# Performance work log

Measured on AMD Instinct MI355X. Metric: run time of the kernel, lower is better.

Reference implementation:

```python
import jax, jax.numpy as jnp
import numpy as np
from jax import lax

B, T, I, H = 8192, 512, 3, 25  # batch, seq_len, input_size, hidden_size


def setup_inputs() -> dict:
    key = jax.random.key(0)
    ks = jax.random.split(key, 4)
    x = jax.random.normal(ks[0], (B, T, I), dtype=jnp.float32)
    # xavier-uniform-ish scale for w_ih, orthogonal-ish (plain normal here) for w_hh
    w_ih = jax.random.normal(ks[1], (4 * H, I), dtype=jnp.float32) * 0.5
    w_hh = jax.random.normal(ks[2], (4 * H, H), dtype=jnp.float32) * 0.2
    b_ih = jnp.zeros((4 * H,), dtype=jnp.float32)
    # PyTorch init in module: forget-gate bias (second quarter) set to 1 on each bias
    b_ih = b_ih.at[H:2 * H].set(1.0)
    b_hh = jnp.zeros((4 * H,), dtype=jnp.float32)
    b_hh = b_hh.at[H:2 * H].set(1.0)
    w_lin = jax.random.normal(ks[3], (1, H), dtype=jnp.float32) * 0.3
    b_lin = jnp.zeros((1,), dtype=jnp.float32)
    return {"x": x, "w_ih": w_ih, "w_hh": w_hh, "b_ih": b_ih, "b_hh": b_hh,
            "w_lin": w_lin, "b_lin": b_lin}


def _lstm_last_h(x, w_ih, w_hh, b_ih, b_hh):
    # x: [B, T, I]; returns final hidden state h_T: [B, H]
    b = b_ih + b_hh  # [4H]
    xT = jnp.swapaxes(x, 0, 1)  # [T, B, I]

    def step(carry, x_t):
        h, c = carry
        gates = x_t @ w_ih.T + h @ w_hh.T + b  # [B, 4H]
        i, f, g, o = jnp.split(gates, 4, axis=-1)  # PyTorch gate order i,f,g,o
        i = jax.nn.sigmoid(i)
        f = jax.nn.sigmoid(f)
        g = jnp.tanh(g)
        o = jax.nn.sigmoid(o)
        c = f * c + i * g
        h = o * jnp.tanh(c)
        return (h, c), None

    h0 = jnp.zeros((x.shape[0], w_hh.shape[1]), dtype=x.dtype)
    (h, _), _ = lax.scan(step, (h0, h0), xT)
    return h


def reference(x, w_ih, w_hh, b_ih, b_hh, w_lin, b_lin):
    h_last = _lstm_last_h(x, w_ih, w_hh, b_ih, b_hh)  # [B, H]
    return h_last @ w_lin.T + b_lin  # [B, 1]
```

## Files before the change

kernel.cpp:

```cpp
#include <hip/hip_runtime.h>
#include <hip/hip_bf16.h>


#define TSTEPS 512
#define ISZ 3
#define HSZ 25

typedef __attribute__((ext_vector_type(8))) short bf16x8;
typedef __attribute__((ext_vector_type(4))) float f32x4;
typedef __attribute__((ext_vector_type(4))) int i32x4;
typedef __attribute__((ext_vector_type(2))) float v2f;

__device__ __forceinline__ unsigned short bf16_bits(float v) {
    return __builtin_bit_cast(unsigned short, __float2bfloat16(v));
}
__device__ __forceinline__ unsigned int pack_bf16(float lo, float hi) {
    return ((unsigned int)bf16_bits(hi) << 16) | (unsigned int)bf16_bits(lo);
}
__device__ __forceinline__ v2f rcp2(v2f v) {
    return (v2f){__builtin_amdgcn_rcpf(v.x), __builtin_amdgcn_rcpf(v.y)};
}

__global__ __launch_bounds__(256, 2) void lstm_mfma(
    const float* __restrict__ x,
    const float* __restrict__ w_ih,
    const float* __restrict__ w_hh,
    const float* __restrict__ b_ih,
    const float* __restrict__ b_hh,
    const float* __restrict__ w_lin,
    const float* __restrict__ b_lin,
    float* __restrict__ out)
{
    __shared__ short hb[2][768];
    __shared__ float outred[4][16];

    const int tid  = threadIdx.x;
    const int w    = tid >> 6;
    const int lane = tid & 63;
    const int n    = lane & 15;
    const int q    = lane >> 4;
    const int b0   = blockIdx.x * 16;

    const float K1 = 1.442695040888963f;
    const float K2 = 2.885390081777927f;

    for (int i = tid; i < 2 * 768; i += 256) ((short*)hb)[i] = 0;

    bf16x8 afA, afB;
    {
        const int g = n & 3, us = n >> 2;
        const int uA = 4 * w + us;
        const int uB = 4 * (w + 4) + us;
        #pragma unroll
        for (int j = 0; j < 8; ++j) {
            const int k = q * 8 + j;
            float vA = 0.f, vB = 0.f;
            {
                const int orow = g * HSZ + uA;
                if (k < ISZ)            vA = w_ih[orow * ISZ + k];
                else if (k == ISZ)      vA = b_ih[orow] + b_hh[orow];
                else if (k < 4 + HSZ)   vA = w_hh[orow * HSZ + (k - 4)];
                vA *= (g == 2) ? -K2 : -K1;
            }
            if (uB < HSZ) {
                const int orow = g * HSZ + uB;
                if (k < ISZ)            vB = w_ih[orow * ISZ + k];
                else if (k == ISZ)      vB = b_ih[orow] + b_hh[orow];
                else if (k < 4 + HSZ)   vB = w_hh[orow * HSZ + (k - 4)];
                vB *= (g == 2) ? -K2 : -K1;
            }
            afA[j] = (short)bf16_bits(vA);
            afB[j] = (short)bf16_bits(vB);
        }
    }

    const int uwA = 4 * w + q;
    const int uwB = 4 * (w + 4) + q;
    const int kwA = uwA + 4, kwB = uwB + 4;
    const int woffA = (kwA >> 3) * 128 + n * 8 + (kwA & 7);
    const int woffB = (kwB >> 3) * 128 + n * 8 + (kwB & 7);
    const int rdoff = lane * 8;

    v2f c = {0.f, 0.f}, h = {0.f, 0.f};

    const float* __restrict__ xg = x + (size_t)(b0 + n) * (TSTEPS * ISZ);
    float4 a0 = ((const float4*)xg)[0];
    float4 a1 = ((const float4*)xg)[1];
    float4 a2 = ((const float4*)xg)[2];

    __syncthreads();

    auto step = [&](int rp, float x0, float x1, float x2) {
        bf16x8 frag = *(const bf16x8*)&hb[rp][rdoff];
        i32x4 fi = __builtin_bit_cast(i32x4, frag);
        const int px0 = (int)pack_bf16(x0, x1);
        const int px1 = (int)pack_bf16(x2, 1.0f);
        fi[0] = (q == 0) ? px0 : fi[0];
        fi[1] = (q == 0) ? px1 : fi[1];
        frag = __builtin_bit_cast(bf16x8, fi);

        const f32x4 zc = {0.f, 0.f, 0.f, 0.f};
        const f32x4 aA = __builtin_amdgcn_mfma_f32_16x16x32_bf16(afA, frag, zc, 0, 0, 0);
        const f32x4 aB = __builtin_amdgcn_mfma_f32_16x16x32_bf16(afB, frag, zc, 0, 0, 0);

        const v2f e0 = {__builtin_amdgcn_exp2f(aA[0]), __builtin_amdgcn_exp2f(aB[0])};
        const v2f e1 = {__builtin_amdgcn_exp2f(aA[1]), __builtin_amdgcn_exp2f(aB[1])};
        const v2f e2 = {__builtin_amdgcn_exp2f(fminf(aA[2], 126.f)),
                        __builtin_amdgcn_exp2f(fminf(aB[2], 126.f))};
        const v2f e3 = {__builtin_amdgcn_exp2f(aA[3]), __builtin_amdgcn_exp2f(aB[3])};
        const v2f one = {1.f, 1.f};
        const v2f s0 = e0 + one, s1 = e1 + one, s2 = e2 + one, m2 = one - e2;
        const v2f p02 = s0 * s2;
        const v2f num = c * p02 + m2 * s1;
        const v2f den = p02 * s1;
        c = num * rcp2(den);
        const v2f ec = {__builtin_amdgcn_exp2f(fminf(-K2 * c.x, 126.f)),
                        __builtin_amdgcn_exp2f(fminf(-K2 * c.y, 126.f))};
        const v2f hden = (e3 + one) * (ec + one);
        h = (one - ec) * rcp2(hden);

        const int wp = rp ^ 1;
        hb[wp][woffA] = (short)bf16_bits(h.x);
        hb[wp][woffB] = (short)bf16_bits(h.y);
        asm volatile("s_waitcnt lgkmcnt(0)" ::: "memory");
        __builtin_amdgcn_s_barrier();
    };

    #pragma unroll 1
    for (int g = 0; g < 128; g += 2) {
        const float4* __restrict__ p1 =
            (const float4*)(xg + (size_t)((g + 1 < 128 ? g + 1 : 127) * 12));
        const float4 n0 = p1[0], n1 = p1[1], n2 = p1[2];
        step(0, a0.x, a0.y, a0.z);
        step(1, a0.w, a1.x, a1.y);
        step(0, a1.z, a1.w, a2.x);
        step(1, a2.y, a2.z, a2.w);
        const float4* __restrict__ p2 =
            (const float4*)(xg + (size_t)((g + 2 < 128 ? g + 2 : 127) * 12));
        a0 = p2[0]; a1 = p2[1]; a2 = p2[2];
        step(0, n0.x, n0.y, n0.z);
        step(1, n0.w, n1.x, n1.y);
        step(0, n1.z, n1.w, n2.x);
        step(1, n2.y, n2.z, n2.w);
    }

    const float wlA = (uwA < HSZ) ? w_lin[uwA] : 0.f;
    const float wlB = (uwB < HSZ) ? w_lin[uwB] : 0.f;
    float v = wlA * h.x + wlB * h.y;
    v += __shfl_xor(v, 16);
    v += __shfl_xor(v, 32);
    if (lane < 16) outred[w][lane] = v;
    __syncthreads();
    if (tid < 16) {
        float s = b_lin[0];
        #pragma unroll
        for (int k2 = 0; k2 < 4; ++k2) s += outred[k2][tid];
        out[b0 + tid] = s;
    }
}

extern "C" void kernel_launch(void* const* d_in, const int* in_sizes, int n_in,
                              void* d_out, int out_size, void* d_ws, size_t ws_size,
                              hipStream_t stream) {
    const float* x     = (const float*)d_in[0];
    const float* w_ih  = (const float*)d_in[1];
    const float* w_hh  = (const float*)d_in[2];
    const float* b_ih  = (const float*)d_in[3];
    const float* b_hh  = (const float*)d_in[4];
    const float* w_lin = (const float*)d_in[5];
    const float* b_lin = (const float*)d_in[6];
    float* out = (float*)d_out;

    lstm_mfma<<<8192 / 16, 256, 0, stream>>>(x, w_ih, w_hh, b_ih, b_hh,
                                             w_lin, b_lin, out);
}
```

Before: 257.5 us.

## Interleave two independent batch chains per block to hide recurrence latency

Each block now handles 32 batch rows as two independent 16-row LSTM chains, interleaving their MFMA and activation work between shared barriers. This halves the number of barriers per unit of work and gives the scheduler independent instructions to cover the serial dependency latency of each step. It halves the grid to 256 blocks, sets launch bounds to one block per SM, and requests 90KB of dynamic shared memory, apparently to force single-block occupancy. That cuts available wave parallelism on a 256-CU device.

```diff
diff --git a/kernel.cpp b/kernel.cpp
--- a/kernel.cpp
+++ b/kernel.cpp
@@ -21,7 +21,7 @@
     return (v2f){__builtin_amdgcn_rcpf(v.x), __builtin_amdgcn_rcpf(v.y)};
 }
 
-__global__ __launch_bounds__(256, 2) void lstm_mfma(
+__global__ __launch_bounds__(256, 1) void lstm_mfma(
     const float* __restrict__ x,
     const float* __restrict__ w_ih,
     const float* __restrict__ w_hh,
@@ -31,20 +31,20 @@
     const float* __restrict__ b_lin,
     float* __restrict__ out)
 {
-    __shared__ short hb[2][768];
-    __shared__ float outred[4][16];
+    __shared__ short hb[2][2][768];
+    __shared__ float outred[4][2][16];
 
     const int tid  = threadIdx.x;
     const int w    = tid >> 6;
     const int lane = tid & 63;
     const int n    = lane & 15;
     const int q    = lane >> 4;
-    const int b0   = blockIdx.x * 16;
+    const int b0   = blockIdx.x * 32;
 
     const float K1 = 1.442695040888963f;
     const float K2 = 2.885390081777927f;
 
-    for (int i = tid; i < 2 * 768; i += 256) ((short*)hb)[i] = 0;
+    for (int i = tid; i < 384; i += 256) ((int4*)hb)[i] = (int4){0, 0, 0, 0};
 
     bf16x8 afA, afB;
     {
@@ -81,17 +81,23 @@
     const int woffB = (kwB >> 3) * 128 + n * 8 + (kwB & 7);
     const int rdoff = lane * 8;
 
-    v2f c = {0.f, 0.f}, h = {0.f, 0.f};
+    v2f c0 = {0.f, 0.f}, h0 = {0.f, 0.f};
+    v2f c1 = {0.f, 0.f}, h1 = {0.f, 0.f};
 
-    const float* __restrict__ xg = x + (size_t)(b0 + n) * (TSTEPS * ISZ);
-    float4 a0 = ((const float4*)xg)[0];
-    float4 a1 = ((const float4*)xg)[1];
-    float4 a2 = ((const float4*)xg)[2];
+    const float* __restrict__ xg0 = x + (size_t)(b0 + n) * (TSTEPS * ISZ);
+    const float* __restrict__ xg1 = x + (size_t)(b0 + 16 + n) * (TSTEPS * ISZ);
+    float4 A0 = ((const float4*)xg0)[0];
+    float4 A1 = ((const float4*)xg0)[1];
+    float4 A2 = ((const float4*)xg0)[2];
+    float4 B0 = ((const float4*)xg1)[0];
+    float4 B1 = ((const float4*)xg1)[1];
+    float4 B2 = ((const float4*)xg1)[2];
 
     __syncthreads();
 
-    auto step = [&](int rp, float x0, float x1, float x2) {
-        bf16x8 frag = *(const bf16x8*)&hb[rp][rdoff];
+    auto chainstep = [&](short (&buf)[2][768], int rp, v2f& c, v2f& h,
+                         float x0, float x1, float x2) {
+        bf16x8 frag = *(const bf16x8*)&buf[rp][rdoff];
         i32x4 fi = __builtin_bit_cast(i32x4, frag);
         const int px0 = (int)pack_bf16(x0, x1);
         const int px1 = (int)pack_bf16(x2, 1.0f);
@@ -120,42 +126,59 @@
         h = (one - ec) * rcp2(hden);
 
         const int wp = rp ^ 1;
-        hb[wp][woffA] = (short)bf16_bits(h.x);
-        hb[wp][woffB] = (short)bf16_bits(h.y);
+        buf[wp][woffA] = (short)bf16_bits(h.x);
+        buf[wp][woffB] = (short)bf16_bits(h.y);
+    };
+
+    auto step2 = [&](int rp, float ax0, float ax1, float ax2,
+                     float bx0, float bx1, float bx2) {
+        chainstep(hb[0], rp, c0, h0, ax0, ax1, ax2);
+        chainstep(hb[1], rp, c1, h1, bx0, bx1, bx2);
         asm volatile("s_waitcnt lgkmcnt(0)" ::: "memory");
         __builtin_amdgcn_s_barrier();
     };
 
     #pragma unroll 1
     for (int g = 0; g < 128; g += 2) {
-        const float4* __restrict__ p1 =
-            (const float4*)(xg + (size_t)((g + 1 < 128 ? g + 1 : 127) * 12));
-        const float4 n0 = p1[0], n1 = p1[1], n2 = p1[2];
-        step(0, a0.x, a0.y, a0.z);
-        step(1, a0.w, a1.x, a1.y);
-        step(0, a1.z, a1.w, a2.x);
-        step(1, a2.y, a2.z, a2.w);
-        const float4* __restrict__ p2 =
-            (const float4*)(xg + (size_t)((g + 2 < 128 ? g + 2 : 127) * 12));
-        a0 = p2[0]; a1 = p2[1]; a2 = p2[2];
-        step(0, n0.x, n0.y, n0.z);
-        step(1, n0.w, n1.x, n1.y);
-        step(0, n1.z, n1.w, n2.x);
-        step(1, n2.y, n2.z, n2.w);
+        const int gp1 = (g + 1 < 128) ? g + 1 : 127;
+        const float4* __restrict__ pA1 = (const float4*)(xg0 + (size_t)gp1 * 12);
+        const float4* __restrict__ pB1 = (const float4*)(xg1 + (size_t)gp1 * 12);
+        const float4 nA0 = pA1[0], nA1 = pA1[1], nA2 = pA1[2];
+        const float4 nB0 = pB1[0], nB1 = pB1[1], nB2 = pB1[2];
+        step2(0, A0.x, A0.y, A0.z, B0.x, B0.y, B0.z);
+        step2(1, A0.w, A1.x, A1.y, B0.w, B1.x, B1.y);
+        step2(0, A1.z, A1.w, A2.x, B1.z, B1.w, B2.x);
+        step2(1, A2.y, A2.z, A2.w, B2.y, B2.z, B2.w);
+        const int gp2 = (g + 2 < 128) ? g + 2 : 127;
+        const float4* __restrict__ pA2 = (const float4*)(xg0 + (size_t)gp2 * 12);
+        const float4* __restrict__ pB2 = (const float4*)(xg1 + (size_t)gp2 * 12);
+        A0 = pA2[0]; A1 = pA2[1]; A2 = pA2[2];
+        B0 = pB2[0]; B1 = pB2[1]; B2 = pB2[2];
+        step2(0, nA0.x, nA0.y, nA0.z, nB0.x, nB0.y, nB0.z);
+        step2(1, nA0.w, nA1.x, nA1.y, nB0.w, nB1.x, nB1.y);
+        step2(0, nA1.z, nA1.w, nA2.x, nB1.z, nB1.w, nB2.x);
+        step2(1, nA2.y, nA2.z, nA2.w, nB2.y, nB2.z, nB2.w);
     }
 
     const float wlA = (uwA < HSZ) ? w_lin[uwA] : 0.f;
     const float wlB = (uwB < HSZ) ? w_lin[uwB] : 0.f;
-    float v = wlA * h.x + wlB * h.y;
-    v += __shfl_xor(v, 16);
-    v += __shfl_xor(v, 32);
-    if (lane < 16) outred[w][lane] = v;
+    float v0 = wlA * h0.x + wlB * h0.y;
+    float v1 = wlA * h1.x + wlB * h1.y;
+    v0 += __shfl_xor(v0, 16);
+    v1 += __shfl_xor(v1, 16);
+    v0 += __shfl_xor(v0, 32);
+    v1 += __shfl_xor(v1, 32);
+    if (lane < 16) {
+        outred[w][0][lane] = v0;
+        outred[w][1][lane] = v1;
+    }
     __syncthreads();
-    if (tid < 16) {
+    if (tid < 32) {
+        const int c2 = tid >> 4, nn = tid & 15;
         float s = b_lin[0];
         #pragma unroll
-        for (int k2 = 0; k2 < 4; ++k2) s += outred[k2][tid];
-        out[b0 + tid] = s;
+        for (int k2 = 0; k2 < 4; ++k2) s += outred[k2][c2][nn];
+        out[b0 + c2 * 16 + nn] = s;
     }
 }
 
@@ -171,6 +194,6 @@
     const float* b_lin = (const float*)d_in[6];
     float* out = (float*)d_out;
 
-    lstm_mfma<<<8192 / 16, 256, 0, stream>>>(x, w_ih, w_hh, b_ih, b_hh,
-                                             w_lin, b_lin, out);
+    lstm_mfma<<<8192 / 32, 256, 90 * 1024, stream>>>(x, w_ih, w_hh, b_ih, b_hh,
+                                                     w_lin, b_lin, out);
 }
```

Result: slower. 349.1 us (+35.6%).
